# Kernel optimization log

Measured on AMD Instinct MI355X. Metric: run time of the kernel, lower is better.

The kernel has to match this reference:

```python
import jax, jax.numpy as jnp
import numpy as np

B, T, HID, D_IN, D_OUT = 64, 4096, 128, 22, 2


def setup_inputs() -> dict:
    key = jax.random.key(0)
    ks = jax.random.split(key, 20)
    s = 1.0 / np.sqrt(HID)
    return {
        "x": jax.random.normal(ks[0], (B, T, 11, 2), jnp.float32),
        "u": jax.random.normal(ks[1], (B, T, 2, 1), jnp.float32),
        "dt": jnp.float32(0.01),
        "theta": jax.random.normal(ks[2], (2, 2), jnp.float32),
        "H_e": jax.random.normal(ks[3], (1,), jnp.float32),
        "tau_e": 1.0 + 0.1 * jax.random.normal(ks[4], (1,), jnp.float32),
        "H_i": jax.random.normal(ks[5], (1,), jnp.float32),
        "tau_i": 1.0 + 0.1 * jax.random.normal(ks[6], (1,), jnp.float32),
        "lam1": jax.random.normal(ks[7], (1,), jnp.float32),
        "lam2": jax.random.normal(ks[8], (1,), jnp.float32),
        "lam3": jax.random.normal(ks[9], (1,), jnp.float32),
        "lam4": jax.random.normal(ks[10], (1,), jnp.float32),
        "C_f": jax.random.normal(ks[11], (2, 2), jnp.float32),
        "C_l": jax.random.normal(ks[12], (2, 2), jnp.float32),
        "C_u": jax.random.normal(ks[13], (2, 2), jnp.float32),
        "C_b": jax.random.normal(ks[14], (2, 2), jnp.float32),
        "W_ih": s * jax.random.normal(ks[15], (4 * HID, D_IN), jnp.float32),
        "W_hh": s * jax.random.normal(ks[16], (4 * HID, HID), jnp.float32),
        "b_ih": s * jax.random.normal(ks[17], (4 * HID,), jnp.float32),
        "b_hh": s * jax.random.normal(ks[18], (4 * HID,), jnp.float32),
        "W_lin": s * jax.random.normal(ks[19], (D_OUT, HID), jnp.float32),
        "b_lin": jnp.zeros((D_OUT,), jnp.float32),
    }


def _forward(x, u, dt, theta, H_e, tau_e, H_i, tau_i, lam1, lam2, lam3, lam4,
             C_f, C_l, C_u, C_b, W_ih, W_hh, b_ih, b_hh, W_lin, b_lin):
    # x: [B,T,11,2] state channels, u: [B,T,2,1] exogenous input.
    # Key insight: the per-step ODE update reads only x[:,t] (the provided
    # trajectory), never the previous ODE output, so it vectorizes over T.
    # Only the LSTM hidden/cell state is truly sequential -> lax.scan.
    sig = jax.nn.sigmoid
    Bb, Tt = x.shape[0], x.shape[1]
    I2 = jnp.eye(2, dtype=x.dtype)
    xt_theta = jnp.einsum('btn,nm->btm', x[:, :, 0, :], theta)   # [B,T,2]
    ut_theta = jnp.einsum('btn,nm->btm', u[..., 0], theta)       # [B,T,2]
    s_xt = sig(xt_theta)
    He_te = H_e / tau_e
    # torch did matmul(M, v.T).T; equivalently v @ M.T (einsum 'btn,mn->btm').
    x0 = x[:, :, 0] + dt * (x[:, :, 5] - x[:, :, 6])
    x1 = x[:, :, 1] + dt * x[:, :, 4]
    x2 = x[:, :, 2] + dt * x[:, :, 5]
    x3 = x[:, :, 3] + dt * x[:, :, 6]
    x4 = x[:, :, 4] + dt * (He_te * (jnp.einsum('btn,mn->btm', s_xt, C_f + C_l + lam1 * I2)
                                     + jnp.einsum('btn,mn->btm', ut_theta, C_u))
                            - 2.0 * x[:, :, 4] / tau_e - x[:, :, 1] / tau_e ** 2)
    x5 = x[:, :, 5] + dt * (He_te * (jnp.einsum('btn,mn->btm', s_xt, C_b + C_l)
                                     + lam2 * sig(x[:, :, 3]))
                            - 2.0 * x[:, :, 5] / tau_e - x[:, :, 2] / tau_e ** 2)
    x6 = x[:, :, 6] + dt * (H_i / tau_i * lam4 * sig(x[:, :, 7])
                            - 2.0 * x[:, :, 6] / tau_i - x[:, :, 3] / tau_i ** 2)
    x7 = x[:, :, 7] + dt * x[:, :, 8]
    x8 = x[:, :, 8] + dt * (He_te * jnp.einsum('btn,mn->btm', s_xt, C_b + C_l + lam3 * I2)
                            - 2.0 * x[:, :, 8] / tau_e - x[:, :, 7] / tau_e ** 2)
    state = jnp.stack([x0, x1, x2, x3, x4, x5, x6, x7, x8,
                       x[:, :, 9], x[:, :, 10]], axis=2)     # [B,T,11,2]
    feats = state.reshape(Bb, Tt, 22)                         # LSTM inputs

    H = W_hh.shape[1]
    # Precompute input-to-gate projection for all steps (one big GEMM).
    gates_in = jnp.einsum('bti,gi->btg', feats, W_ih) + b_ih + b_hh  # [B,T,4H]

    def step(carry, g_in):
        h, c = carry
        g = g_in + h @ W_hh.T                                 # [B,4H]
        i = sig(g[:, :H])
        f = sig(g[:, H:2 * H])
        gg = jnp.tanh(g[:, 2 * H:3 * H])
        o = sig(g[:, 3 * H:])
        c = f * c + i * gg
        h = o * jnp.tanh(c)
        return (h, c), h

    h0 = jnp.zeros((Bb, H), feats.dtype)
    _, hs = jax.lax.scan(step, (h0, h0), jnp.swapaxes(gates_in, 0, 1))
    hs = jnp.swapaxes(hs, 0, 1)                               # [B,T,H]
    out = jnp.einsum('bth,oh->bto', hs, W_lin) + b_lin        # [B,T,2]
    return out[..., None]                                     # [B,T,2,1]


def reference(x, u, dt, theta, H_e, tau_e, H_i, tau_i, lam1, lam2, lam3, lam4,
              C_f, C_l, C_u, C_b, W_ih, W_hh, b_ih, b_hh, W_lin, b_lin):
    return _forward(x, u, dt, theta, H_e, tau_e, H_i, tau_i, lam1, lam2, lam3, lam4,
                    C_f, C_l, C_u, C_b, W_ih, W_hh, b_ih, b_hh, W_lin, b_lin)
```

## Files before the change

kernel.cpp:

```cpp
#include <hip/hip_runtime.h>

#define B_   64
#define T_   4096
#define HID_ 128

typedef float f32x4 __attribute__((ext_vector_type(4)));
typedef short s16x8 __attribute__((ext_vector_type(8)));
typedef short s16x4 __attribute__((ext_vector_type(4)));

__device__ __forceinline__ float fexp2(float x){ float r; asm("v_exp_f32 %0, %1":"=v"(r):"v"(x)); return r; }
__device__ __forceinline__ float frcp (float x){ float r; asm("v_rcp_f32 %0, %1":"=v"(r):"v"(x)); return r; }
__device__ __forceinline__ unsigned short f2bf(float f){
    unsigned u = __float_as_uint(f);
    u += 0x7FFFu + ((u >> 16) & 1u);
    return (unsigned short)(u >> 16);
}
__device__ __forceinline__ float sigf(float x){
    return frcp(1.0f + fexp2(-1.44269504089f * x));
}
__device__ __forceinline__ void bar_lgkm(){
    asm volatile("s_waitcnt lgkmcnt(0)\ns_barrier" ::: "memory");
    __builtin_amdgcn_sched_barrier(0);
}

__global__ __launch_bounds__(256) void k_feats(
    const float* __restrict__ x, const float* __restrict__ u,
    const float* __restrict__ dtp, const float* __restrict__ theta,
    const float* __restrict__ He, const float* __restrict__ taue,
    const float* __restrict__ Hi, const float* __restrict__ taui,
    const float* __restrict__ l1, const float* __restrict__ l2,
    const float* __restrict__ l3, const float* __restrict__ l4,
    const float* __restrict__ Cf, const float* __restrict__ Cl,
    const float* __restrict__ Cu, const float* __restrict__ Cb,
    unsigned short* __restrict__ feats)
{
    long idx = (long)blockIdx.x * 256 + threadIdx.x;
    const float dt = dtp[0];
    const float th00 = theta[0], th01 = theta[1], th10 = theta[2], th11 = theta[3];
    const float he = He[0], te = taue[0], hi = Hi[0], ti = taui[0];
    const float L1 = l1[0], L2v = l2[0], L3 = l3[0], L4 = l4[0];
    float cf[4], cl[4], cu[4], cb[4];
    #pragma unroll
    for (int i = 0; i < 4; ++i){ cf[i]=Cf[i]; cl[i]=Cl[i]; cu[i]=Cu[i]; cb[i]=Cb[i]; }
    const float ite  = 1.f/te, iti = 1.f/ti;
    const float He_te = he*ite, ite2 = ite*ite;
    const float Hi_ti = hi*iti, iti2 = iti*iti;

    float X[22];
    const float2* xr = (const float2*)(x + idx*22);
    #pragma unroll
    for (int i = 0; i < 11; ++i){ float2 v = xr[i]; X[2*i] = v.x; X[2*i+1] = v.y; }
    float2 uv = ((const float2*)u)[idx];

    float xt0 = X[0]*th00 + X[1]*th10;
    float xt1 = X[0]*th01 + X[1]*th11;
    float ut0 = uv.x*th00 + uv.y*th10;
    float ut1 = uv.x*th01 + uv.y*th11;
    float s0 = sigf(xt0), s1 = sigf(xt1);

    float Mf00 = cf[0]+cl[0]+L1, Mf01 = cf[1]+cl[1], Mf10 = cf[2]+cl[2], Mf11 = cf[3]+cl[3]+L1;
    float Af0 = Mf00*s0 + Mf01*s1, Af1 = Mf10*s0 + Mf11*s1;
    float Au0 = cu[0]*ut0 + cu[1]*ut1, Au1 = cu[2]*ut0 + cu[3]*ut1;
    float Mb00 = cb[0]+cl[0], Mb01 = cb[1]+cl[1], Mb10 = cb[2]+cl[2], Mb11 = cb[3]+cl[3];
    float Abl0 = Mb00*s0 + Mb01*s1, Abl1 = Mb10*s0 + Mb11*s1;
    float A30 = (Mb00+L3)*s0 + Mb01*s1,  A31 = Mb10*s0 + (Mb11+L3)*s1;

    float F[22];
    F[0]  = X[0]  + dt*(X[10]-X[12]);
    F[1]  = X[1]  + dt*(X[11]-X[13]);
    F[2]  = X[2]  + dt*X[8];
    F[3]  = X[3]  + dt*X[9];
    F[4]  = X[4]  + dt*X[10];
    F[5]  = X[5]  + dt*X[11];
    F[6]  = X[6]  + dt*X[12];
    F[7]  = X[7]  + dt*X[13];
    F[8]  = X[8]  + dt*(He_te*(Af0+Au0) - 2.f*X[8]*ite  - X[2]*ite2);
    F[9]  = X[9]  + dt*(He_te*(Af1+Au1) - 2.f*X[9]*ite  - X[3]*ite2);
    F[10] = X[10] + dt*(He_te*(Abl0 + L2v*sigf(X[6])) - 2.f*X[10]*ite - X[4]*ite2);
    F[11] = X[11] + dt*(He_te*(Abl1 + L2v*sigf(X[7])) - 2.f*X[11]*ite - X[5]*ite2);
    F[12] = X[12] + dt*(Hi_ti*L4*sigf(X[14]) - 2.f*X[12]*iti - X[6]*iti2);
    F[13] = X[13] + dt*(Hi_ti*L4*sigf(X[15]) - 2.f*X[13]*iti - X[7]*iti2);
    F[14] = X[14] + dt*X[16];
    F[15] = X[15] + dt*X[17];
    F[16] = X[16] + dt*(He_te*A30 - 2.f*X[16]*ite - X[14]*ite2);
    F[17] = X[17] + dt*(He_te*A31 - 2.f*X[17]*ite - X[15]*ite2);
    F[18] = X[18]; F[19] = X[19]; F[20] = X[20]; F[21] = X[21];

    unsigned short op[32];
    #pragma unroll
    for (int s = 0; s < 4; ++s){
        #pragma unroll
        for (int e = 0; e < 8; ++e){
            int j = s*4 + (e & 3) + ((e >> 2) << 4);
            op[s*8+e] = (j < 22) ? f2bf(F[j]) : (unsigned short)0;
        }
    }
    uint4* dst = (uint4*)(feats + idx*32);
    #pragma unroll
    for (int q = 0; q < 4; ++q){
        uint4 v;
        v.x = (unsigned)op[q*8+0] | ((unsigned)op[q*8+1] << 16);
        v.y = (unsigned)op[q*8+2] | ((unsigned)op[q*8+3] << 16);
        v.z = (unsigned)op[q*8+4] | ((unsigned)op[q*8+5] << 16);
        v.w = (unsigned)op[q*8+6] | ((unsigned)op[q*8+7] << 16);
        dst[q] = v;
    }
}

__global__ __launch_bounds__(512, 1) void k_scan(
    const unsigned short* __restrict__ feats,
    const float* __restrict__ Wih, const float* __restrict__ Whh,
    const float* __restrict__ bih, const float* __restrict__ bhh,
    const float* __restrict__ Wlin, const float* __restrict__ blin,
    float* __restrict__ out)
{
    __shared__ __align__(16) unsigned short hist[16 * 576];
    __shared__ __align__(16) unsigned short fch[64 * 32];
    __shared__ __align__(16) float gfb[64 * 512];

    const int tid = threadIdx.x;
    const int w  = tid >> 6;
    const int l  = tid & 63;
    const int lm = l & 15;
    const int lg = l >> 4;
    const int gb0 = blockIdx.x * 4;
    const int ar  = lm >> 2;

    for (int i = tid; i < 16*576/2; i += 512) ((unsigned*)hist)[i] = 0u;

    const int nj = w*16 + lm;
    s16x8 bw[4][5];
    #pragma unroll
    for (int t4 = 0; t4 < 4; ++t4){
        int n = t4*128 + nj;
        #pragma unroll
        for (int kc = 0; kc < 5; ++kc){
            #pragma unroll
            for (int j = 0; j < 8; ++j){
                int k = kc*32 + lg*4 + (j & 3) + ((j >> 2) << 4);
                float wv = 0.f;
                if (kc == 0){ if (k < 22) wv = Wih[n*22 + k]; }
                else        { wv = Whh[n*128 + (k - 32)]; }
                bw[t4][kc][j] = (short)f2bf(wv);
            }
        }
    }
    s16x8 wlf[4];
    #pragma unroll
    for (int kc = 0; kc < 4; ++kc){
        #pragma unroll
        for (int j = 0; j < 8; ++j){
            int k = kc*32 + lg*4 + (j & 3) + ((j >> 2) << 4);
            wlf[kc][j] = (lm < 2) ? (short)f2bf(Wlin[lm*128 + k]) : (short)0;
        }
    }
    const float blv = blin[l & 1];

    const float L2E = 1.44269504089f;
    float nLb0, nLb1, nLb3, b2g;
    {
        float bi = bih[0*128+nj] + bhh[0*128+nj];
        float bf = bih[1*128+nj] + bhh[1*128+nj];
        float bg = bih[2*128+nj] + bhh[2*128+nj];
        float bo = bih[3*128+nj] + bhh[3*128+nj];
        nLb0 = -L2E*bi; nLb1 = -L2E*bf; nLb3 = -L2E*bo; b2g = 2.f*L2E*bg;
    }

    const int aoff = ar*144 + lg*8;
    const int khc = nj >> 5;
    const int hwoff = lg*144 + (khc*4 + ((nj >> 2) & 3))*8 + ((nj >> 4) & 1)*4 + (nj & 3);

    const float* gfr0 = gfb + lg*512 + nj*4;
    const float* gfr8 = gfr0 + 8*2048;
    float* gw0 = gfb + (lg*4)*512 + nj*4;
    float* gw2 = gw0 + 32*512;

    const int u_t = tid >> 4, u_b = (tid >> 2) & 3, u_q = tid & 3;
    const unsigned short* psrc = feats + ((long)(gb0 + u_b)*T_ + u_t)*32 + u_q*8;
    unsigned short* const pdst = fch + (u_t*4 + u_b)*32 + u_q*8;

    uint4 pend = {0,0,0,0};
    if (tid < 256) pend = *(const uint4*)psrc;

    __syncthreads();

    const f32x4 Z4 = {0.f, 0.f, 0.f, 0.f};
    float c = 0.f;

    for (int chk = 0; chk < T_/16; ++chk){
        if (tid < 256) *(uint4*)pdst = pend;
        bar_lgkm();
        {
            long nk = (chk < T_/16 - 1) ? (chk + 1) : chk;
            if (tid < 256) pend = *(const uint4*)(psrc + nk*16*32);
        }
        #pragma unroll
        for (int mt = 0; mt < 4; ++mt){
            const unsigned short* ap = fch + (mt*16 + (lm>>2)*4 + (lm&3))*32 + lg*8;
            s16x8 af = *(const s16x8*)ap;
            f32x4 m0 = __builtin_amdgcn_mfma_f32_16x16x32_bf16(af, bw[0][0], Z4, 0,0,0);
            f32x4 m1 = __builtin_amdgcn_mfma_f32_16x16x32_bf16(af, bw[1][0], Z4, 0,0,0);
            f32x4 m2 = __builtin_amdgcn_mfma_f32_16x16x32_bf16(af, bw[2][0], Z4, 0,0,0);
            f32x4 m3 = __builtin_amdgcn_mfma_f32_16x16x32_bf16(af, bw[3][0], Z4, 0,0,0);
            float* gw = (mt < 2) ? gw0 : gw2;
            const int mo = (mt & 1) * 16;
            #pragma unroll
            for (int r = 0; r < 4; ++r){
                f32x4 v = {m0[r], m1[r], m2[r], m3[r]};
                *(f32x4*)(gw + (mo + r)*512) = v;
            }
        }
        if (w >= 4 && chk > 0){
            const int mt = w - 4;
            const unsigned short* ap = hist + (mt*4 + (lm>>2))*576 + (lm&3)*144 + lg*8;
            s16x8 q0 = *(const s16x8*)(ap +  0);
            s16x8 q1 = *(const s16x8*)(ap + 32);
            s16x8 q2 = *(const s16x8*)(ap + 64);
            s16x8 q3 = *(const s16x8*)(ap + 96);
            f32x4 acc = __builtin_amdgcn_mfma_f32_16x16x32_bf16(q0, wlf[0], Z4, 0,0,0);
            acc = __builtin_amdgcn_mfma_f32_16x16x32_bf16(q1, wlf[1], acc, 0,0,0);
            acc = __builtin_amdgcn_mfma_f32_16x16x32_bf16(q2, wlf[2], acc, 0,0,0);
            acc = __builtin_amdgcn_mfma_f32_16x16x32_bf16(q3, wlf[3], acc, 0,0,0);
            if (lm < 2){
                const int tY = (chk - 1)*16 + mt*4 + lg;
                #pragma unroll
                for (int r = 0; r < 4; ++r)
                    out[((long)(gb0 + r)*T_ + tY)*2 + lm] = acc[r] + blv;
            }
        }
        bar_lgkm();

        #pragma unroll
        for (int s = 0; s < 16; ++s){
            const int p = (s + 15) & 15;
            const unsigned short* hp = hist + p*576 + aoff;
            s16x8 h1 = *(const s16x8*)(hp +  0);
            s16x8 h2 = *(const s16x8*)(hp + 32);
            s16x8 h3 = *(const s16x8*)(hp + 64);
            s16x8 h4 = *(const s16x8*)(hp + 96);
            f32x4 gf = *(const f32x4*)(((s < 8) ? gfr0 : gfr8) + (s & 7)*2048);

            f32x4 a0 = __builtin_amdgcn_mfma_f32_16x16x32_bf16(h1, bw[0][1], Z4, 0,0,0);
            f32x4 a1 = __builtin_amdgcn_mfma_f32_16x16x32_bf16(h1, bw[1][1], Z4, 0,0,0);
            f32x4 a2 = __builtin_amdgcn_mfma_f32_16x16x32_bf16(h1, bw[2][1], Z4, 0,0,0);
            f32x4 a3 = __builtin_amdgcn_mfma_f32_16x16x32_bf16(h1, bw[3][1], Z4, 0,0,0);
            a0 = __builtin_amdgcn_mfma_f32_16x16x32_bf16(h2, bw[0][2], a0, 0,0,0);
            a1 = __builtin_amdgcn_mfma_f32_16x16x32_bf16(h2, bw[1][2], a1, 0,0,0);
            a2 = __builtin_amdgcn_mfma_f32_16x16x32_bf16(h2, bw[2][2], a2, 0,0,0);
            a3 = __builtin_amdgcn_mfma_f32_16x16x32_bf16(h2, bw[3][2], a3, 0,0,0);
            a0 = __builtin_amdgcn_mfma_f32_16x16x32_bf16(h3, bw[0][3], a0, 0,0,0);
            a1 = __builtin_amdgcn_mfma_f32_16x16x32_bf16(h3, bw[1][3], a1, 0,0,0);
            a2 = __builtin_amdgcn_mfma_f32_16x16x32_bf16(h3, bw[2][3], a2, 0,0,0);
            a3 = __builtin_amdgcn_mfma_f32_16x16x32_bf16(h3, bw[3][3], a3, 0,0,0);
            a0 = __builtin_amdgcn_mfma_f32_16x16x32_bf16(h4, bw[0][4], a0, 0,0,0);
            a1 = __builtin_amdgcn_mfma_f32_16x16x32_bf16(h4, bw[1][4], a1, 0,0,0);
            a2 = __builtin_amdgcn_mfma_f32_16x16x32_bf16(h4, bw[2][4], a2, 0,0,0);
            a3 = __builtin_amdgcn_mfma_f32_16x16x32_bf16(h4, bw[3][4], a3, 0,0,0);

            float gi = a0[0] + gf[0];
            float gfo = a1[0] + gf[1];
            float gg = a2[0] + gf[2];
            float go = a3[0] + gf[3];
            float si = frcp(1.f + fexp2(fmaf(gi,  -L2E, nLb0)));
            float sf = frcp(1.f + fexp2(fmaf(gfo, -L2E, nLb1)));
            float so = frcp(1.f + fexp2(fmaf(go,  -L2E, nLb3)));
            float eg = fexp2(fmaf(gg, 2.f*L2E, b2g));
            float tg_ = fmaf(-2.f, frcp(1.f + eg), 1.f);
            c = sf*c + si*tg_;
            float ec = fexp2(c * (2.f*L2E));
            float tc_ = fmaf(-2.f, frcp(1.f + ec), 1.f);
            float h = so * tc_;

            unsigned hp2;
            asm("v_cvt_pk_bf16_f32 %0, %1, %1" : "=v"(hp2) : "v"(h));
            hist[s*576 + hwoff] = (unsigned short)hp2;

            bar_lgkm();
        }
    }

    if (w >= 4){
        const int mt = w - 4;
        const unsigned short* ap = hist + (mt*4 + (lm>>2))*576 + (lm&3)*144 + lg*8;
        s16x8 q0 = *(const s16x8*)(ap +  0);
        s16x8 q1 = *(const s16x8*)(ap + 32);
        s16x8 q2 = *(const s16x8*)(ap + 64);
        s16x8 q3 = *(const s16x8*)(ap + 96);
        f32x4 acc = __builtin_amdgcn_mfma_f32_16x16x32_bf16(q0, wlf[0], Z4, 0,0,0);
        acc = __builtin_amdgcn_mfma_f32_16x16x32_bf16(q1, wlf[1], acc, 0,0,0);
        acc = __builtin_amdgcn_mfma_f32_16x16x32_bf16(q2, wlf[2], acc, 0,0,0);
        acc = __builtin_amdgcn_mfma_f32_16x16x32_bf16(q3, wlf[3], acc, 0,0,0);
        if (lm < 2){
            const int tY = (T_ - 16) + mt*4 + lg;
            #pragma unroll
            for (int r = 0; r < 4; ++r)
                out[((long)(gb0 + r)*T_ + tY)*2 + lm] = acc[r] + blv;
        }
    }
}

extern "C" void kernel_launch(void* const* d_in, const int* in_sizes, int n_in,
                              void* d_out, int out_size, void* d_ws, size_t ws_size,
                              hipStream_t stream)
{
    const float* x     = (const float*)d_in[0];
    const float* u     = (const float*)d_in[1];
    const float* dtp   = (const float*)d_in[2];
    const float* theta = (const float*)d_in[3];
    const float* He    = (const float*)d_in[4];
    const float* taue  = (const float*)d_in[5];
    const float* Hi    = (const float*)d_in[6];
    const float* taui  = (const float*)d_in[7];
    const float* l1    = (const float*)d_in[8];
    const float* l2    = (const float*)d_in[9];
    const float* l3    = (const float*)d_in[10];
    const float* l4    = (const float*)d_in[11];
    const float* Cf    = (const float*)d_in[12];
    const float* Cl    = (const float*)d_in[13];
    const float* Cu    = (const float*)d_in[14];
    const float* Cb    = (const float*)d_in[15];
    const float* Wih   = (const float*)d_in[16];
    const float* Whh   = (const float*)d_in[17];
    const float* bih   = (const float*)d_in[18];
    const float* bhh   = (const float*)d_in[19];
    const float* Wlin  = (const float*)d_in[20];
    const float* blin  = (const float*)d_in[21];

    unsigned short* feats = (unsigned short*)d_ws;

    k_feats<<<(B_*T_)/256, 256, 0, stream>>>(x,u,dtp,theta,He,taue,Hi,taui,
                                             l1,l2,l3,l4,Cf,Cl,Cu,Cb,feats);
    k_scan<<<16, 512, 0, stream>>>(feats, Wih, Whh, bih, bhh, Wlin, blin, (float*)d_out);
}
```

Before: 1.896 ms.

## Interleave next-chunk input projection MFMAs into the sequential LSTM step loop

Moves the per-chunk input-to-gate MFMA projection out of its own phase and spreads it across the 16 recurrent steps, one MFMA per step, writing results one step later so they fill idle matrix-unit slots in the latency-bound recurrence. The first chunk is precomputed before the loop, and feature prefetch now runs two chunks ahead. The gate buffer row stride is padded from 512 to 516 floats, presumably to reduce LDS bank conflicts. This adds LDS scalar stores and register pressure inside the critical step loop, and the software pipeline needs correct prologue and boundary handling.

```diff
diff --git a/kernel.cpp b/kernel.cpp
--- a/kernel.cpp
+++ b/kernel.cpp
@@ -116,7 +116,7 @@
 {
     __shared__ __align__(16) unsigned short hist[16 * 576];
     __shared__ __align__(16) unsigned short fch[64 * 32];
-    __shared__ __align__(16) float gfb[64 * 512];
+    __shared__ __align__(16) float gfb[64 * 516];
 
     const int tid = threadIdx.x;
     const int w  = tid >> 6;
@@ -169,47 +169,41 @@
     const int aoff = ar*144 + lg*8;
     const int khc = nj >> 5;
     const int hwoff = lg*144 + (khc*4 + ((nj >> 2) & 3))*8 + ((nj >> 4) & 1)*4 + (nj & 3);
-
-    const float* gfr0 = gfb + lg*512 + nj*4;
-    const float* gfr8 = gfr0 + 8*2048;
-    float* gw0 = gfb + (lg*4)*512 + nj*4;
-    float* gw2 = gw0 + 32*512;
+    const float* gfrB = gfb + lg*516 + nj*4;
+    float* const gwB  = gfb + (4*lg)*516 + nj*4;
 
     const int u_t = tid >> 4, u_b = (tid >> 2) & 3, u_q = tid & 3;
     const unsigned short* psrc = feats + ((long)(gb0 + u_b)*T_ + u_t)*32 + u_q*8;
     unsigned short* const pdst = fch + (u_t*4 + u_b)*32 + u_q*8;
 
+    const f32x4 Z4 = {0.f, 0.f, 0.f, 0.f};
+
+    if (tid < 256){ uint4 t0 = *(const uint4*)psrc; *(uint4*)pdst = t0; }
+    __syncthreads();
+    #pragma unroll
+    for (int mt = 0; mt < 4; ++mt){
+        s16x8 af = *(const s16x8*)(fch + (mt*16 + lm)*32 + lg*8);
+        f32x4 m0 = __builtin_amdgcn_mfma_f32_16x16x32_bf16(af, bw[0][0], Z4, 0,0,0);
+        f32x4 m1 = __builtin_amdgcn_mfma_f32_16x16x32_bf16(af, bw[1][0], Z4, 0,0,0);
+        f32x4 m2 = __builtin_amdgcn_mfma_f32_16x16x32_bf16(af, bw[2][0], Z4, 0,0,0);
+        f32x4 m3 = __builtin_amdgcn_mfma_f32_16x16x32_bf16(af, bw[3][0], Z4, 0,0,0);
+        #pragma unroll
+        for (int r = 0; r < 4; ++r){
+            f32x4 v = {m0[r], m1[r], m2[r], m3[r]};
+            *(f32x4*)(gwB + (16*mt + r)*516) = v;
+        }
+    }
     uint4 pend = {0,0,0,0};
-    if (tid < 256) pend = *(const uint4*)psrc;
-
+    if (tid < 256) pend = *(const uint4*)(psrc + (long)1*16*32);
     __syncthreads();
 
-    const f32x4 Z4 = {0.f, 0.f, 0.f, 0.f};
+    f32x4 p[4] = {Z4, Z4, Z4, Z4};
+    s16x8 afg = {0,0,0,0,0,0,0,0};
     float c = 0.f;
-
-    for (int chk = 0; chk < T_/16; ++chk){
+    const int NCHK = T_/16;
+
+    for (int chk = 0; chk < NCHK; ++chk){
         if (tid < 256) *(uint4*)pdst = pend;
-        bar_lgkm();
-        {
-            long nk = (chk < T_/16 - 1) ? (chk + 1) : chk;
-            if (tid < 256) pend = *(const uint4*)(psrc + nk*16*32);
-        }
-        #pragma unroll
-        for (int mt = 0; mt < 4; ++mt){
-            const unsigned short* ap = fch + (mt*16 + (lm>>2)*4 + (lm&3))*32 + lg*8;
-            s16x8 af = *(const s16x8*)ap;
-            f32x4 m0 = __builtin_amdgcn_mfma_f32_16x16x32_bf16(af, bw[0][0], Z4, 0,0,0);
-            f32x4 m1 = __builtin_amdgcn_mfma_f32_16x16x32_bf16(af, bw[1][0], Z4, 0,0,0);
-            f32x4 m2 = __builtin_amdgcn_mfma_f32_16x16x32_bf16(af, bw[2][0], Z4, 0,0,0);
-            f32x4 m3 = __builtin_amdgcn_mfma_f32_16x16x32_bf16(af, bw[3][0], Z4, 0,0,0);
-            float* gw = (mt < 2) ? gw0 : gw2;
-            const int mo = (mt & 1) * 16;
-            #pragma unroll
-            for (int r = 0; r < 4; ++r){
-                f32x4 v = {m0[r], m1[r], m2[r], m3[r]};
-                *(f32x4*)(gw + (mo + r)*512) = v;
-            }
-        }
         if (w >= 4 && chk > 0){
             const int mt = w - 4;
             const unsigned short* ap = hist + (mt*4 + (lm>>2))*576 + (lm&3)*144 + lg*8;
@@ -229,16 +223,34 @@
             }
         }
         bar_lgkm();
+        {
+            long nk = (chk < NCHK-2) ? (chk + 2) : (NCHK-1);
+            if (tid < 256) pend = *(const uint4*)(psrc + nk*16*32);
+        }
+        afg = *(const s16x8*)(fch + (0*16 + lm)*32 + lg*8);
 
         #pragma unroll
         for (int s = 0; s < 16; ++s){
-            const int p = (s + 15) & 15;
-            const unsigned short* hp = hist + p*576 + aoff;
+            {
+                const int mt_w = (s >= 4) ? ((s-4) >> 2) : 3;
+                const int g_w  = (s >= 4) ? ((s-4) & 3) : s;
+                if (s >= 4 || chk > 0){
+                    float* wp = gwB + 16*mt_w*516 + g_w;
+                    wp[0*516] = p[s&3][0]; wp[1*516] = p[s&3][1];
+                    wp[2*516] = p[s&3][2]; wp[3*516] = p[s&3][3];
+                }
+            }
+            p[s&3] = __builtin_amdgcn_mfma_f32_16x16x32_bf16(afg, bw[s&3][0], Z4, 0,0,0);
+
+            const unsigned short* hp = hist + ((s+15)&15)*576 + aoff;
             s16x8 h1 = *(const s16x8*)(hp +  0);
             s16x8 h2 = *(const s16x8*)(hp + 32);
             s16x8 h3 = *(const s16x8*)(hp + 64);
             s16x8 h4 = *(const s16x8*)(hp + 96);
-            f32x4 gf = *(const f32x4*)(((s < 8) ? gfr0 : gfr8) + (s & 7)*2048);
+            f32x4 gf = *(const f32x4*)(gfrB + s*4*516);
+
+            if ((s & 3) == 3 && s < 15)
+                afg = *(const s16x8*)(fch + (((s>>2)+1)*16 + lm)*32 + lg*8);
 
             f32x4 a0 = __builtin_amdgcn_mfma_f32_16x16x32_bf16(h1, bw[0][1], Z4, 0,0,0);
             f32x4 a1 = __builtin_amdgcn_mfma_f32_16x16x32_bf16(h1, bw[1][1], Z4, 0,0,0);
@@ -257,10 +269,10 @@
             a2 = __builtin_amdgcn_mfma_f32_16x16x32_bf16(h4, bw[2][4], a2, 0,0,0);
             a3 = __builtin_amdgcn_mfma_f32_16x16x32_bf16(h4, bw[3][4], a3, 0,0,0);
 
-            float gi = a0[0] + gf[0];
+            float gi  = a0[0] + gf[0];
             float gfo = a1[0] + gf[1];
-            float gg = a2[0] + gf[2];
-            float go = a3[0] + gf[3];
+            float gg  = a2[0] + gf[2];
+            float go  = a3[0] + gf[3];
             float si = frcp(1.f + fexp2(fmaf(gi,  -L2E, nLb0)));
             float sf = frcp(1.f + fexp2(fmaf(gfo, -L2E, nLb1)));
             float so = frcp(1.f + fexp2(fmaf(go,  -L2E, nLb3)));
```

New measurement: 1.930 ms. Within noise of the previous version (+1.8%).

## Keep input-gate MFMA results in registers instead of LDS staging buffer

Applied to the files above, without the earlier changes.

Removes the 128KB shared gfb buffer. Each chunk's input projection MFMA results now stay in registers (p[4][4]), with the A-operand layout remapped so each step's row lands in the right accumulator lane. The feature prefetch becomes two chunks deep and the fch write moves after the barrier. This saves LDS writes and reads per chunk and frees LDS, at the cost of 64 more VGPRs and new ordering assumptions around the fch buffer.

```diff
diff --git a/kernel.cpp b/kernel.cpp
--- a/kernel.cpp
+++ b/kernel.cpp
@@ -116,7 +116,6 @@
 {
     __shared__ __align__(16) unsigned short hist[16 * 576];
     __shared__ __align__(16) unsigned short fch[64 * 32];
-    __shared__ __align__(16) float gfb[64 * 512];
 
     const int tid = threadIdx.x;
     const int w  = tid >> 6;
@@ -169,46 +168,38 @@
     const int aoff = ar*144 + lg*8;
     const int khc = nj >> 5;
     const int hwoff = lg*144 + (khc*4 + ((nj >> 2) & 3))*8 + ((nj >> 4) & 1)*4 + (nj & 3);
-
-    const float* gfr0 = gfb + lg*512 + nj*4;
-    const float* gfr8 = gfr0 + 8*2048;
-    float* gw0 = gfb + (lg*4)*512 + nj*4;
-    float* gw2 = gw0 + 32*512;
+    const int gfoff = ((lm & 3)*4 + (lm >> 2))*32 + lg*8;
 
     const int u_t = tid >> 4, u_b = (tid >> 2) & 3, u_q = tid & 3;
     const unsigned short* psrc = feats + ((long)(gb0 + u_b)*T_ + u_t)*32 + u_q*8;
     unsigned short* const pdst = fch + (u_t*4 + u_b)*32 + u_q*8;
 
+    const f32x4 Z4 = {0.f, 0.f, 0.f, 0.f};
+
+    if (tid < 256){ uint4 t0 = *(const uint4*)psrc; *(uint4*)pdst = t0; }
     uint4 pend = {0,0,0,0};
-    if (tid < 256) pend = *(const uint4*)psrc;
-
+    if (tid < 256) pend = *(const uint4*)(psrc + (long)16*32);
     __syncthreads();
 
-    const f32x4 Z4 = {0.f, 0.f, 0.f, 0.f};
+    f32x4 p[4][4];
     float c = 0.f;
-
-    for (int chk = 0; chk < T_/16; ++chk){
-        if (tid < 256) *(uint4*)pdst = pend;
+    const int NCHK = T_/16;
+
+    for (int chk = 0; chk < NCHK; ++chk){
+        #pragma unroll
+        for (int mt = 0; mt < 4; ++mt){
+            s16x8 af = *(const s16x8*)(fch + mt*16*32 + gfoff);
+            p[mt][0] = __builtin_amdgcn_mfma_f32_16x16x32_bf16(af, bw[0][0], Z4, 0,0,0);
+            p[mt][1] = __builtin_amdgcn_mfma_f32_16x16x32_bf16(af, bw[1][0], Z4, 0,0,0);
+            p[mt][2] = __builtin_amdgcn_mfma_f32_16x16x32_bf16(af, bw[2][0], Z4, 0,0,0);
+            p[mt][3] = __builtin_amdgcn_mfma_f32_16x16x32_bf16(af, bw[3][0], Z4, 0,0,0);
+        }
         bar_lgkm();
-        {
-            long nk = (chk < T_/16 - 1) ? (chk + 1) : chk;
-            if (tid < 256) pend = *(const uint4*)(psrc + nk*16*32);
-        }
-        #pragma unroll
-        for (int mt = 0; mt < 4; ++mt){
-            const unsigned short* ap = fch + (mt*16 + (lm>>2)*4 + (lm&3))*32 + lg*8;
-            s16x8 af = *(const s16x8*)ap;
-            f32x4 m0 = __builtin_amdgcn_mfma_f32_16x16x32_bf16(af, bw[0][0], Z4, 0,0,0);
-            f32x4 m1 = __builtin_amdgcn_mfma_f32_16x16x32_bf16(af, bw[1][0], Z4, 0,0,0);
-            f32x4 m2 = __builtin_amdgcn_mfma_f32_16x16x32_bf16(af, bw[2][0], Z4, 0,0,0);
-            f32x4 m3 = __builtin_amdgcn_mfma_f32_16x16x32_bf16(af, bw[3][0], Z4, 0,0,0);
-            float* gw = (mt < 2) ? gw0 : gw2;
-            const int mo = (mt & 1) * 16;
-            #pragma unroll
-            for (int r = 0; r < 4; ++r){
-                f32x4 v = {m0[r], m1[r], m2[r], m3[r]};
-                *(f32x4*)(gw + (mo + r)*512) = v;
-            }
+
+        if (tid < 256){
+            *(uint4*)pdst = pend;
+            long nk = (chk < NCHK-2) ? (chk + 2) : (NCHK-1);
+            pend = *(const uint4*)(psrc + nk*16*32);
         }
         if (w >= 4 && chk > 0){
             const int mt = w - 4;
@@ -232,13 +223,11 @@
 
         #pragma unroll
         for (int s = 0; s < 16; ++s){
-            const int p = (s + 15) & 15;
-            const unsigned short* hp = hist + p*576 + aoff;
+            const unsigned short* hp = hist + ((s+15)&15)*576 + aoff;
             s16x8 h1 = *(const s16x8*)(hp +  0);
             s16x8 h2 = *(const s16x8*)(hp + 32);
             s16x8 h3 = *(const s16x8*)(hp + 64);
             s16x8 h4 = *(const s16x8*)(hp + 96);
-            f32x4 gf = *(const f32x4*)(((s < 8) ? gfr0 : gfr8) + (s & 7)*2048);
 
             f32x4 a0 = __builtin_amdgcn_mfma_f32_16x16x32_bf16(h1, bw[0][1], Z4, 0,0,0);
             f32x4 a1 = __builtin_amdgcn_mfma_f32_16x16x32_bf16(h1, bw[1][1], Z4, 0,0,0);
@@ -257,10 +246,10 @@
             a2 = __builtin_amdgcn_mfma_f32_16x16x32_bf16(h4, bw[2][4], a2, 0,0,0);
             a3 = __builtin_amdgcn_mfma_f32_16x16x32_bf16(h4, bw[3][4], a3, 0,0,0);
 
-            float gi = a0[0] + gf[0];
-            float gfo = a1[0] + gf[1];
-            float gg = a2[0] + gf[2];
-            float go = a3[0] + gf[3];
+            float gi  = a0[0] + p[s>>2][0][s&3];
+            float gfo = a1[0] + p[s>>2][1][s&3];
+            float gg  = a2[0] + p[s>>2][2][s&3];
+            float go  = a3[0] + p[s>>2][3][s&3];
             float si = frcp(1.f + fexp2(fmaf(gi,  -L2E, nLb0)));
             float sf = frcp(1.f + fexp2(fmaf(gfo, -L2E, nLb1)));
             float so = frcp(1.f + fexp2(fmaf(go,  -L2E, nLb3)));
```

Result: faster. 1.768 ms (-6.8%).
